# Kernel tuning notes

Hardware: AMD Instinct MI355X
Metric: run time of the kernel (lower is better)

Reference implementation:

```python
import jax, jax.numpy as jnp
import numpy as np

N_NODES = 50000
N_EDGES = 800000
IN_C = 128
OUT_C = 128
EDGE_F = 16
NEG_SLOPE = 0.2
BN_EPS = 1e-5


def setup_inputs() -> dict:
    key = jax.random.key(0)
    ks = jax.random.split(key, 8)
    x = jax.random.normal(ks[0], (N_NODES, IN_C), dtype=jnp.float32)
    edge_index = jax.random.randint(ks[1], (2, N_EDGES), 0, N_NODES, dtype=jnp.int64)
    edge_attr = jax.random.normal(ks[2], (N_EDGES, EDGE_F), dtype=jnp.float32)
    W = jax.random.normal(ks[3], (IN_C, OUT_C), dtype=jnp.float32) / np.sqrt(IN_C)
    att_src = jax.random.normal(ks[4], (OUT_C,), dtype=jnp.float32) / np.sqrt(OUT_C)
    att_dst = jax.random.normal(ks[5], (OUT_C,), dtype=jnp.float32) / np.sqrt(OUT_C)
    bias = jnp.zeros((OUT_C,), dtype=jnp.float32)
    gamma = jnp.ones((OUT_C,), dtype=jnp.float32)
    beta = jnp.zeros((OUT_C,), dtype=jnp.float32)
    return {"x": x, "edge_index": edge_index, "edge_attr": edge_attr, "W": W,
            "att_src": att_src, "att_dst": att_dst, "bias": bias,
            "gamma": gamma, "beta": beta}


def reference(x, edge_index, edge_attr, W, att_src, att_dst, bias, gamma, beta):
    # GATConv, heads=1, concat=False; edge_attr is ignored (edge_dim=None in original).
    N = x.shape[0]
    h = x @ W  # [N, C] linear projection (shared lin_src/lin_dst)
    # add self loops (PyG default add_self_loops=True)
    loops = jnp.broadcast_to(jnp.arange(N, dtype=edge_index.dtype)[None, :], (2, N))
    ei = jnp.concatenate([edge_index, loops], axis=1)
    src, dst = ei[0], ei[1]
    a_src = h @ att_src  # [N] per-node source attention logit
    a_dst = h @ att_dst  # [N] per-node target attention logit
    e = jax.nn.leaky_relu(a_src[src] + a_dst[dst], NEG_SLOPE)  # [E+N]
    # segment softmax over edges grouped by destination node
    m = jax.ops.segment_max(e, dst, num_segments=N)  # every node has a self loop -> nonempty
    ex = jnp.exp(e - m[dst])
    denom = jax.ops.segment_sum(ex, dst, num_segments=N)
    alpha = ex / denom[dst]  # [E+N]
    out = jax.ops.segment_sum(alpha[:, None] * h[src], dst, num_segments=N) + bias  # [N, C]
    # NodeLevelBatchNorm in training mode: batch stats over nodes, biased variance
    mean = jnp.mean(out, axis=0)
    var = jnp.mean((out - mean) ** 2, axis=0)
    y = (out - mean) * jax.lax.rsqrt(var + BN_EPS) * gamma + beta
    return jax.nn.relu(y)
```

## Files before the change

kernel.cpp:

```cpp
#include <hip/hip_runtime.h>
#include <hip/hip_bf16.h>

#define NN 50000
#define NE 800000
#define NC 128
#define NEG 0.2f
#define BN_EPS 1e-5f
#define NB 391
#define EPB 2048
#define DEPTH 16
#define CAP 2560
#define GB 391
#define AGGB 2048

typedef unsigned int u32;
typedef unsigned short u16;
typedef short bf16x8 __attribute__((ext_vector_type(8)));
typedef float f32x4 __attribute__((ext_vector_type(4)));

#define OFF_H       0
#define OFF_ACCUM   3200000
#define OFF_ASRC    6400000
#define OFF_ADST    6450000
#define OFF_GCUR    6500000
#define OFF_GSUM    6500512
#define OFF_GSUMSQ  6500640
#define OFF_BEG     6500768
#define OFF_ENDA    6550768
#define OFF_ESRC    6600768
#define OFF_WGT     7601728
#define OFF_BIN     8602688
#define OFF_WB      9603648
#define OFF_PS      9611840
#define OFF_PQ      9873984
#define OFF_WSEND   10136128
#define NZERO       512

__device__ __forceinline__ float leaky(float e) { return (e >= 0.f) ? e : NEG * e; }

__device__ __forceinline__ u16 f2b(float f) {
  union { float f; u32 u; } v; v.f = f;
  u32 u = v.u;
  return (u16)((u + 0x7fffu + ((u >> 16) & 1u)) >> 16);
}
__device__ __forceinline__ float blo(u32 u) {
  union { u32 u; float f; } v; v.u = u << 16; return v.f;
}
__device__ __forceinline__ float bhi(u32 u) {
  union { u32 u; float f; } v; v.u = u & 0xffff0000u; return v.f;
}

__device__ __forceinline__ bool ei_is64(const void* ei_raw) {
  const unsigned long long* p64 = (const unsigned long long*)ei_raw;
  bool is64 = true;
#pragma unroll
  for (int k = 0; k < 8; ++k) is64 = is64 && (p64[k] < (unsigned long long)NN);
  return is64;
}

__global__ __launch_bounds__(256) void k_prep(
    const float* __restrict__ W, u32* __restrict__ Wb32, int* __restrict__ zbase) {
  if (blockIdx.x == 0) {
    for (int i = threadIdx.x; i < NZERO; i += 256) zbase[i] = 0;
  }
  int q = blockIdx.x * 256 + threadIdx.x;
  if (q >= 2048) return;
  int f = q >> 6, l = q & 63;
  int n = f >> 2, s = f & 3;
  int col = 16 * n + (l & 15);
  int kb = 32 * s + 8 * (l >> 4);
#pragma unroll
  for (int j2 = 0; j2 < 4; ++j2) {
    u16 e0 = f2b(W[(kb + 2 * j2) * NC + col]);
    u16 e1 = f2b(W[(kb + 2 * j2 + 1) * NC + col]);
    Wb32[q * 4 + j2] = ((u32)e1 << 16) | e0;
  }
}

__global__ __launch_bounds__(256) void k_gemm_bin(
    const float* __restrict__ x, const u16* __restrict__ Wb,
    const float* __restrict__ attS, const float* __restrict__ attD,
    u16* __restrict__ h, float* __restrict__ a_src, float* __restrict__ a_dst,
    const void* __restrict__ ei_raw, int* __restrict__ gcur, u32* __restrict__ bin) {
  __shared__ int cnt[NB];
  __shared__ u32 buf[NB * DEPTH];
  const int t = threadIdx.x;

  if (blockIdx.x >= GB) {
    for (int i = t; i < NB; i += 256) cnt[i] = 0;
    __syncthreads();
    bool is64 = ei_is64(ei_raw);
    int base = (blockIdx.x - GB) * EPB;
#pragma unroll
    for (int k = 0; k < 8; ++k) {
      int idx = base + k * 256 + t;
      if (idx >= NE) continue;
      int s, d;
      if (is64) {
        s = (int)((const long long*)ei_raw)[idx];
        d = (int)((const long long*)ei_raw)[NE + idx];
      } else {
        s = ((const int*)ei_raw)[idx];
        d = ((const int*)ei_raw)[NE + idx];
      }
      int b = d >> 7;
      u32 pack = (u32)s | ((u32)(d & 127) << 16);
      int p = atomicAdd(&cnt[b], 1);
      if (p < DEPTH) buf[b * DEPTH + p] = pack;
      else {
        int g = atomicAdd(&gcur[b], 1);
        if (g < CAP) bin[b * CAP + g] = pack;
      }
    }
    __syncthreads();
    for (int b = t; b < NB; b += 256) {
      int c = min(cnt[b], DEPTH);
      if (c > 0) {
        int g = atomicAdd(&gcur[b], c);
        int lim = min(c, max(0, CAP - g));
        int gp = b * CAP + g;
#pragma unroll 4
        for (int i = 0; i < lim; ++i) bin[gp + i] = buf[b * DEPTH + i];
      }
    }
    return;
  }

  const int l = t & 63;
  const int r0 = blockIdx.x * 128 + (t >> 6) * 32;
  const int lr = l & 15;
  const int kg = l >> 4;

  f32x4 acc[2][8];
#pragma unroll
  for (int t2 = 0; t2 < 2; ++t2)
#pragma unroll
    for (int n = 0; n < 8; ++n) acc[t2][n] = (f32x4){0.f, 0.f, 0.f, 0.f};

#pragma unroll
  for (int s = 0; s < 4; ++s) {
    bf16x8 bfr[8];
#pragma unroll
    for (int n = 0; n < 8; ++n)
      bfr[n] = *(const bf16x8*)(Wb + ((size_t)((n * 4 + s) * 64 + l)) * 8);

#pragma unroll
    for (int t2 = 0; t2 < 2; ++t2) {
      int arow = r0 + t2 * 16 + lr;
      f32x4 a0 = (f32x4){0.f,0.f,0.f,0.f}, a1 = a0;
      if (arow < NN) {
        const float* xa = x + (size_t)arow * NC + kg * 8 + s * 32;
        a0 = *(const f32x4*)xa;
        a1 = *(const f32x4*)(xa + 4);
      }
      bf16x8 af;
      af[0]=(short)f2b(a0[0]); af[1]=(short)f2b(a0[1]);
      af[2]=(short)f2b(a0[2]); af[3]=(short)f2b(a0[3]);
      af[4]=(short)f2b(a1[0]); af[5]=(short)f2b(a1[1]);
      af[6]=(short)f2b(a1[2]); af[7]=(short)f2b(a1[3]);
#pragma unroll
      for (int n = 0; n < 8; ++n)
        acc[t2][n] = __builtin_amdgcn_mfma_f32_16x16x32_bf16(af, bfr[n], acc[t2][n], 0, 0, 0);
    }
  }

  float attS_r[8], attD_r[8];
#pragma unroll
  for (int n = 0; n < 8; ++n) {
    attS_r[n] = attS[16 * n + lr];
    attD_r[n] = attD[16 * n + lr];
  }
#pragma unroll
  for (int t2 = 0; t2 < 2; ++t2) {
#pragma unroll
    for (int q = 0; q < 4; ++q) {
      int row = r0 + t2 * 16 + kg * 4 + q;
      bool rok = row < NN;
      float sA = 0.f, sD = 0.f;
#pragma unroll
      for (int n = 0; n < 8; ++n) {
        float v = acc[t2][n][q];
        sA += v * attS_r[n];
        sD += v * attD_r[n];
        if (rok) h[(size_t)row * NC + 16 * n + lr] = f2b(v);
      }
      sA += __shfl_xor(sA, 1); sD += __shfl_xor(sD, 1);
      sA += __shfl_xor(sA, 2); sD += __shfl_xor(sD, 2);
      sA += __shfl_xor(sA, 4); sD += __shfl_xor(sD, 4);
      sA += __shfl_xor(sA, 8); sD += __shfl_xor(sD, 8);
      if (lr == 0 && rok) { a_src[row] = sA; a_dst[row] = sD; }
    }
  }
}

__global__ __launch_bounds__(256) void k_build(
    const int* __restrict__ gcur, const u32* __restrict__ bin,
    const float* __restrict__ a_src, const float* __restrict__ a_dst,
    int* __restrict__ begA, int* __restrict__ endA,
    int* __restrict__ esrc, float* __restrict__ wgt) {
  __shared__ int cnt[128], bs[128], cur[128];
  __shared__ float aDl[128];
  int t = threadIdx.x;
  int b = blockIdx.x;
  int nbase = b << 7;
  int nmax = min(128, NN - nbase);
  int ebeg = b * CAP;
  int E = min(gcur[b], CAP);
  if (t < 128) { cnt[t] = 0; if (t < nmax) aDl[t] = a_dst[nbase + t]; }
  __syncthreads();
  for (int i = t; i < E; i += 256)
    atomicAdd(&cnt[bin[ebeg + i] >> 16], 1);
  __syncthreads();
  if (t < 128) bs[t] = cnt[t];
  __syncthreads();
  for (int off = 1; off < 128; off <<= 1) {
    int xv = (t < 128 && t >= off) ? bs[t - off] : 0;
    __syncthreads();
    if (t < 128) bs[t] += xv;
    __syncthreads();
  }
  if (t < 128) {
    int ex = bs[t] - cnt[t];
    bs[t] = ex;
    cur[t] = 0;
    if (t < nmax) {
      begA[nbase + t] = ebeg + ex;
      endA[nbase + t] = ebeg + ex + cnt[t];
    }
  }
  __syncthreads();
  for (int i = t; i < E; i += 256) {
    u32 e = bin[ebeg + i];
    int s = e & 0xFFFF;
    int ld = e >> 16;
    int p = atomicAdd(&cur[ld], 1);
    int pos = ebeg + bs[ld] + p;
    esrc[pos] = s;
    wgt[pos] = __expf(leaky(a_src[s] + aDl[ld]));
  }
}

__global__ __launch_bounds__(256) void k_aggregate(
    const int* __restrict__ begA, const int* __restrict__ endA,
    const int* __restrict__ esrc, const float* __restrict__ wgt,
    const float* __restrict__ a_src, const float* __restrict__ a_dst,
    const u16* __restrict__ h, u32* __restrict__ accum,
    float* __restrict__ partS, float* __restrict__ partQ) {
  int t = threadIdx.x;
  int l = t & 63;
  int wv = t >> 6;
  float cs0 = 0.f, cs1 = 0.f, cq0 = 0.f, cq1 = 0.f;

  for (int d = blockIdx.x * 4 + wv; d < NN; d += AGGB * 4) {
    int beg = begA[d], end = endA[d];

    float2 ac0 = make_float2(0.f, 0.f), ac1 = ac0, ac2 = ac0, ac3 = ac0;
    float wpart = 0.f;

    for (int j0 = beg; j0 < end; j0 += 64) {
      int n = min(64, end - j0);
      int s = 0;
      float w = 0.f;
      if (l < n) {
        s = esrc[j0 + l];
        w = wgt[j0 + l];
        wpart += w;
      }
      int jj = 0;
      for (; jj + 8 <= n; jj += 8) {
        int s0 = __shfl(s, jj),     s1 = __shfl(s, jj + 1);
        int s2 = __shfl(s, jj + 2), s3 = __shfl(s, jj + 3);
        int s4 = __shfl(s, jj + 4), s5 = __shfl(s, jj + 5);
        int s6 = __shfl(s, jj + 6), s7 = __shfl(s, jj + 7);
        float w0 = __shfl(w, jj),     w1 = __shfl(w, jj + 1);
        float w2 = __shfl(w, jj + 2), w3 = __shfl(w, jj + 3);
        float w4 = __shfl(w, jj + 4), w5 = __shfl(w, jj + 5);
        float w6 = __shfl(w, jj + 6), w7 = __shfl(w, jj + 7);
        u32 h0 = *(const u32*)&h[(size_t)s0 * NC + 2 * l];
        u32 h1 = *(const u32*)&h[(size_t)s1 * NC + 2 * l];
        u32 h2 = *(const u32*)&h[(size_t)s2 * NC + 2 * l];
        u32 h3 = *(const u32*)&h[(size_t)s3 * NC + 2 * l];
        u32 h4 = *(const u32*)&h[(size_t)s4 * NC + 2 * l];
        u32 h5 = *(const u32*)&h[(size_t)s5 * NC + 2 * l];
        u32 h6 = *(const u32*)&h[(size_t)s6 * NC + 2 * l];
        u32 h7 = *(const u32*)&h[(size_t)s7 * NC + 2 * l];
        ac0.x += w0 * blo(h0); ac0.y += w0 * bhi(h0);
        ac1.x += w1 * blo(h1); ac1.y += w1 * bhi(h1);
        ac2.x += w2 * blo(h2); ac2.y += w2 * bhi(h2);
        ac3.x += w3 * blo(h3); ac3.y += w3 * bhi(h3);
        ac0.x += w4 * blo(h4); ac0.y += w4 * bhi(h4);
        ac1.x += w5 * blo(h5); ac1.y += w5 * bhi(h5);
        ac2.x += w6 * blo(h6); ac2.y += w6 * bhi(h6);
        ac3.x += w7 * blo(h7); ac3.y += w7 * bhi(h7);
      }
      for (; jj + 4 <= n; jj += 4) {
        int s0 = __shfl(s, jj),     s1 = __shfl(s, jj + 1);
        int s2 = __shfl(s, jj + 2), s3 = __shfl(s, jj + 3);
        float w0 = __shfl(w, jj),     w1 = __shfl(w, jj + 1);
        float w2 = __shfl(w, jj + 2), w3 = __shfl(w, jj + 3);
        u32 h0 = *(const u32*)&h[(size_t)s0 * NC + 2 * l];
        u32 h1 = *(const u32*)&h[(size_t)s1 * NC + 2 * l];
        u32 h2 = *(const u32*)&h[(size_t)s2 * NC + 2 * l];
        u32 h3 = *(const u32*)&h[(size_t)s3 * NC + 2 * l];
        ac0.x += w0 * blo(h0); ac0.y += w0 * bhi(h0);
        ac1.x += w1 * blo(h1); ac1.y += w1 * bhi(h1);
        ac2.x += w2 * blo(h2); ac2.y += w2 * bhi(h2);
        ac3.x += w3 * blo(h3); ac3.y += w3 * bhi(h3);
      }
      for (; jj < n; ++jj) {
        int sj = __shfl(s, jj);
        float wj = __shfl(w, jj);
        u32 hw = *(const u32*)&h[(size_t)sj * NC + 2 * l];
        ac0.x += wj * blo(hw); ac0.y += wj * bhi(hw);
      }
    }

    for (int off = 32; off > 0; off >>= 1) wpart += __shfl_xor(wpart, off);

    float wself = __expf(leaky(a_src[d] + a_dst[d]));
    u32 hw = *(const u32*)&h[(size_t)d * NC + 2 * l];
    float accx = ac0.x + ac1.x + ac2.x + ac3.x + wself * blo(hw);
    float accy = ac0.y + ac1.y + ac2.y + ac3.y + wself * bhi(hw);

    float inv = 1.f / (wpart + wself);
    float ox = accx * inv, oy = accy * inv;
    accum[(size_t)d * 64 + l] = ((u32)f2b(oy) << 16) | f2b(ox);
    cs0 += ox; cs1 += oy;
    cq0 += ox * ox; cq1 += oy * oy;
  }

  __shared__ float2 shS[256], shQ[256];
  shS[t] = make_float2(cs0, cs1);
  shQ[t] = make_float2(cq0, cq1);
  __syncthreads();
  if (t < 64) {
    float2 a = shS[t], b = shQ[t];
#pragma unroll
    for (int g = 1; g < 4; ++g) {
      float2 s2v = shS[g * 64 + t], q2 = shQ[g * 64 + t];
      a.x += s2v.x; a.y += s2v.y;
      b.x += q2.x;  b.y += q2.y;
    }
    partS[blockIdx.x * 128 + 2 * t]     = a.x;
    partS[blockIdx.x * 128 + 2 * t + 1] = a.y;
    partQ[blockIdx.x * 128 + 2 * t]     = b.x;
    partQ[blockIdx.x * 128 + 2 * t + 1] = b.y;
  }
}

__global__ __launch_bounds__(256) void k_stats2(
    const float* __restrict__ partS, const float* __restrict__ partQ,
    float* __restrict__ gsum, float* __restrict__ gsumsq) {
  __shared__ float shw[4];
  int t = threadIdx.x;
  int b = blockIdx.x;
  int c = b & 127;
  const float* src = (b >> 7) ? partQ : partS;
  float a = 0.f;
#pragma unroll
  for (int i = t; i < AGGB; i += 256) a += src[(size_t)i * 128 + c];
  for (int off = 32; off > 0; off >>= 1) a += __shfl_xor(a, off);
  if ((t & 63) == 0) shw[t >> 6] = a;
  __syncthreads();
  if (t == 0) {
    float r = shw[0] + shw[1] + shw[2] + shw[3];
    if (b >> 7) gsumsq[c] = r;
    else        gsum[c] = r;
  }
}

__global__ __launch_bounds__(256) void k_bn(
    const u32* __restrict__ accum, const float* __restrict__ gsum,
    const float* __restrict__ gsumsq, const float* __restrict__ gamma,
    const float* __restrict__ beta, float* __restrict__ out) {
  int i4 = blockIdx.x * 256 + threadIdx.x;
  if (i4 >= NN * NC / 4) return;
  int c4 = (i4 * 4) & 127;
  f32x4 gs = *(const f32x4*)&gsum[c4];
  f32x4 gq = *(const f32x4*)&gsumsq[c4];
  f32x4 ga = *(const f32x4*)&gamma[c4];
  f32x4 be = *(const f32x4*)&beta[c4];
  u32 p0 = accum[(size_t)i4 * 2];
  u32 p1 = accum[(size_t)i4 * 2 + 1];
  f32x4 v = (f32x4){blo(p0), bhi(p0), blo(p1), bhi(p1)};
  f32x4 o;
#pragma unroll
  for (int j = 0; j < 4; ++j) {
    float mean = gs[j] * (1.0f / NN);
    float var = gq[j] * (1.0f / NN) - mean * mean;
    float inv = rsqrtf(var + BN_EPS);
    float y = (v[j] - mean) * inv * ga[j] + be[j];
    o[j] = (y > 0.f) ? y : 0.f;
  }
  *(f32x4*)&out[(size_t)i4 * 4] = o;
}

extern "C" void kernel_launch(void* const* d_in, const int* in_sizes, int n_in,
                              void* d_out, int out_size, void* d_ws, size_t ws_size,
                              hipStream_t stream) {
  const float* x    = (const float*)d_in[0];
  const void*  ei   = d_in[1];
  const float* W    = (const float*)d_in[3];
  const float* attS = (const float*)d_in[4];
  const float* attD = (const float*)d_in[5];
  const float* gamma = (const float*)d_in[7];
  const float* beta  = (const float*)d_in[8];

  float* ws     = (float*)d_ws;
  u16*   h      = (u16*)(ws + OFF_H);
  u32*   accum  = (u32*)(ws + OFF_ACCUM);
  float* a_src  = ws + OFF_ASRC;
  float* a_dst  = ws + OFF_ADST;
  int*   gcur   = (int*)(ws + OFF_GCUR);
  float* gsum   = ws + OFF_GSUM;
  float* gsumsq = ws + OFF_GSUMSQ;
  int*   begA   = (int*)(ws + OFF_BEG);
  int*   endA   = (int*)(ws + OFF_ENDA);
  int*   esrc   = (int*)(ws + OFF_ESRC);
  float* wgt    = ws + OFF_WGT;
  u32*   bin    = (u32*)(ws + OFF_BIN);
  u32*   wb32   = (u32*)(ws + OFF_WB);
  float* partS  = ws + OFF_PS;
  float* partQ  = ws + OFF_PQ;

  const int nbin = (NE + EPB - 1) / EPB;
  k_prep<<<8, 256, 0, stream>>>(W, wb32, gcur);
  k_gemm_bin<<<GB + nbin, 256, 0, stream>>>(x, (const u16*)wb32, attS, attD,
                                            h, a_src, a_dst, ei, gcur, bin);
  k_build<<<NB, 256, 0, stream>>>(gcur, bin, a_src, a_dst, begA, endA, esrc, wgt);
  k_aggregate<<<AGGB, 256, 0, stream>>>(begA, endA, esrc, wgt, a_src, a_dst, h,
                                        accum, partS, partQ);
  k_stats2<<<256, 256, 0, stream>>>(partS, partQ, gsum, gsumsq);
  k_bn<<<(NN * NC / 4 + 255) / 256, 256, 0, stream>>>(accum, gsum, gsumsq, gamma, beta,
                                                      (float*)d_out);
}
```

Measured before the change: 103.3 us.

## Interleave edge src/weight records, fold self-loop and softmax denominator into build

The build kernel now writes interleaved (src, weight) records with the self-loop appended to each node's segment. It also accumulates the per-node weight sum in shared memory and stores its reciprocal. The aggregate kernel then streams the records with uniform (scalar) loads instead of lane loads plus shuffles, and drops the cross-lane reduction and self-loop special case. This adds shared-memory float atomics to the build kernel and extra padded capacity per bin.

Result: faster. 90.93 us (-12.0%).

```diff
diff --git a/kernel.cpp b/kernel.cpp
--- a/kernel.cpp
+++ b/kernel.cpp
@@ -10,6 +10,7 @@
 #define EPB 2048
 #define DEPTH 16
 #define CAP 2560
+#define CAPR 2688
 #define GB 391
 #define AGGB 2048
 
@@ -27,13 +28,13 @@
 #define OFF_GSUMSQ  6500640
 #define OFF_BEG     6500768
 #define OFF_ENDA    6550768
-#define OFF_ESRC    6600768
-#define OFF_WGT     7601728
-#define OFF_BIN     8602688
-#define OFF_WB      9603648
-#define OFF_PS      9611840
-#define OFF_PQ      9873984
-#define OFF_WSEND   10136128
+#define OFF_WINV    6600768
+#define OFF_BIN     6650768
+#define OFF_REC     7651728
+#define OFF_WB      9753744
+#define OFF_PS      9761936
+#define OFF_PQ      10024080
+#define OFF_WSEND   10286224
 #define NZERO       512
 
 __device__ __forceinline__ float leaky(float e) { return (e >= 0.f) ? e : NEG * e; }
@@ -196,17 +197,21 @@
 __global__ __launch_bounds__(256) void k_build(
     const int* __restrict__ gcur, const u32* __restrict__ bin,
     const float* __restrict__ a_src, const float* __restrict__ a_dst,
-    int* __restrict__ begA, int* __restrict__ endA,
-    int* __restrict__ esrc, float* __restrict__ wgt) {
+    int* __restrict__ begA, int* __restrict__ endA, float* __restrict__ winv,
+    u32* __restrict__ rec) {
   __shared__ int cnt[128], bs[128], cur[128];
-  __shared__ float aDl[128];
+  __shared__ float aDl[128], wsh[128];
   int t = threadIdx.x;
   int b = blockIdx.x;
   int nbase = b << 7;
   int nmax = min(128, NN - nbase);
   int ebeg = b * CAP;
+  int rbeg = b * CAPR;
   int E = min(gcur[b], CAP);
-  if (t < 128) { cnt[t] = 0; if (t < nmax) aDl[t] = a_dst[nbase + t]; }
+  if (t < 128) {
+    cnt[t] = 0; wsh[t] = 0.f;
+    if (t < nmax) aDl[t] = a_dst[nbase + t];
+  }
   __syncthreads();
   for (int i = t; i < E; i += 256)
     atomicAdd(&cnt[bin[ebeg + i] >> 16], 1);
@@ -220,13 +225,8 @@
     __syncthreads();
   }
   if (t < 128) {
-    int ex = bs[t] - cnt[t];
-    bs[t] = ex;
+    bs[t] -= cnt[t];
     cur[t] = 0;
-    if (t < nmax) {
-      begA[nbase + t] = ebeg + ex;
-      endA[nbase + t] = ebeg + ex + cnt[t];
-    }
   }
   __syncthreads();
   for (int i = t; i < E; i += 256) {
@@ -234,100 +234,77 @@
     int s = e & 0xFFFF;
     int ld = e >> 16;
     int p = atomicAdd(&cur[ld], 1);
-    int pos = ebeg + bs[ld] + p;
-    esrc[pos] = s;
-    wgt[pos] = __expf(leaky(a_src[s] + aDl[ld]));
+    int pos = rbeg + bs[ld] + ld + p;
+    float w = __expf(leaky(a_src[s] + aDl[ld]));
+    rec[2 * pos] = (u32)s;
+    rec[2 * pos + 1] = __float_as_uint(w);
+    atomicAdd(&wsh[ld], w);
+  }
+  __syncthreads();
+  if (t < nmax) {
+    int node = nbase + t;
+    int bg = rbeg + bs[t] + t;
+    int cn = cnt[t];
+    float wself = __expf(leaky(a_src[node] + aDl[t]));
+    rec[2 * (bg + cn)] = (u32)node;
+    rec[2 * (bg + cn) + 1] = __float_as_uint(wself);
+    begA[node] = bg;
+    endA[node] = bg + cn + 1;
+    winv[node] = 1.f / (wsh[t] + wself);
   }
 }
 
 __global__ __launch_bounds__(256) void k_aggregate(
     const int* __restrict__ begA, const int* __restrict__ endA,
-    const int* __restrict__ esrc, const float* __restrict__ wgt,
-    const float* __restrict__ a_src, const float* __restrict__ a_dst,
+    const u32* __restrict__ rec, const float* __restrict__ winv,
     const u16* __restrict__ h, u32* __restrict__ accum,
     float* __restrict__ partS, float* __restrict__ partQ) {
   int t = threadIdx.x;
   int l = t & 63;
   int wv = t >> 6;
+  const u32* h32 = (const u32*)h;
+  const uint2* rec2 = (const uint2*)rec;
   float cs0 = 0.f, cs1 = 0.f, cq0 = 0.f, cq1 = 0.f;
 
+#define P1(EJ, A)                                                          \
+  {                                                                        \
+    int sj = __builtin_amdgcn_readfirstlane((int)(EJ).x);                  \
+    float wj = __uint_as_float((EJ).y);                                    \
+    u32 g = h32[(size_t)sj * 64 + l];                                      \
+    A.x += wj * blo(g);                                                    \
+    A.y += wj * bhi(g);                                                    \
+  }
+
   for (int d = blockIdx.x * 4 + wv; d < NN; d += AGGB * 4) {
-    int beg = begA[d], end = endA[d];
-
-    float2 ac0 = make_float2(0.f, 0.f), ac1 = ac0, ac2 = ac0, ac3 = ac0;
-    float wpart = 0.f;
-
-    for (int j0 = beg; j0 < end; j0 += 64) {
-      int n = min(64, end - j0);
-      int s = 0;
-      float w = 0.f;
-      if (l < n) {
-        s = esrc[j0 + l];
-        w = wgt[j0 + l];
-        wpart += w;
-      }
-      int jj = 0;
-      for (; jj + 8 <= n; jj += 8) {
-        int s0 = __shfl(s, jj),     s1 = __shfl(s, jj + 1);
-        int s2 = __shfl(s, jj + 2), s3 = __shfl(s, jj + 3);
-        int s4 = __shfl(s, jj + 4), s5 = __shfl(s, jj + 5);
-        int s6 = __shfl(s, jj + 6), s7 = __shfl(s, jj + 7);
-        float w0 = __shfl(w, jj),     w1 = __shfl(w, jj + 1);
-        float w2 = __shfl(w, jj + 2), w3 = __shfl(w, jj + 3);
-        float w4 = __shfl(w, jj + 4), w5 = __shfl(w, jj + 5);
-        float w6 = __shfl(w, jj + 6), w7 = __shfl(w, jj + 7);
-        u32 h0 = *(const u32*)&h[(size_t)s0 * NC + 2 * l];
-        u32 h1 = *(const u32*)&h[(size_t)s1 * NC + 2 * l];
-        u32 h2 = *(const u32*)&h[(size_t)s2 * NC + 2 * l];
-        u32 h3 = *(const u32*)&h[(size_t)s3 * NC + 2 * l];
-        u32 h4 = *(const u32*)&h[(size_t)s4 * NC + 2 * l];
-        u32 h5 = *(const u32*)&h[(size_t)s5 * NC + 2 * l];
-        u32 h6 = *(const u32*)&h[(size_t)s6 * NC + 2 * l];
-        u32 h7 = *(const u32*)&h[(size_t)s7 * NC + 2 * l];
-        ac0.x += w0 * blo(h0); ac0.y += w0 * bhi(h0);
-        ac1.x += w1 * blo(h1); ac1.y += w1 * bhi(h1);
-        ac2.x += w2 * blo(h2); ac2.y += w2 * bhi(h2);
-        ac3.x += w3 * blo(h3); ac3.y += w3 * bhi(h3);
-        ac0.x += w4 * blo(h4); ac0.y += w4 * bhi(h4);
-        ac1.x += w5 * blo(h5); ac1.y += w5 * bhi(h5);
-        ac2.x += w6 * blo(h6); ac2.y += w6 * bhi(h6);
-        ac3.x += w7 * blo(h7); ac3.y += w7 * bhi(h7);
-      }
-      for (; jj + 4 <= n; jj += 4) {
-        int s0 = __shfl(s, jj),     s1 = __shfl(s, jj + 1);
-        int s2 = __shfl(s, jj + 2), s3 = __shfl(s, jj + 3);
-        float w0 = __shfl(w, jj),     w1 = __shfl(w, jj + 1);
-        float w2 = __shfl(w, jj + 2), w3 = __shfl(w, jj + 3);
-        u32 h0 = *(const u32*)&h[(size_t)s0 * NC + 2 * l];
-        u32 h1 = *(const u32*)&h[(size_t)s1 * NC + 2 * l];
-        u32 h2 = *(const u32*)&h[(size_t)s2 * NC + 2 * l];
-        u32 h3 = *(const u32*)&h[(size_t)s3 * NC + 2 * l];
-        ac0.x += w0 * blo(h0); ac0.y += w0 * bhi(h0);
-        ac1.x += w1 * blo(h1); ac1.y += w1 * bhi(h1);
-        ac2.x += w2 * blo(h2); ac2.y += w2 * bhi(h2);
-        ac3.x += w3 * blo(h3); ac3.y += w3 * bhi(h3);
-      }
-      for (; jj < n; ++jj) {
-        int sj = __shfl(s, jj);
-        float wj = __shfl(w, jj);
-        u32 hw = *(const u32*)&h[(size_t)sj * NC + 2 * l];
-        ac0.x += wj * blo(hw); ac0.y += wj * bhi(hw);
-      }
-    }
-
-    for (int off = 32; off > 0; off >>= 1) wpart += __shfl_xor(wpart, off);
-
-    float wself = __expf(leaky(a_src[d] + a_dst[d]));
-    u32 hw = *(const u32*)&h[(size_t)d * NC + 2 * l];
-    float accx = ac0.x + ac1.x + ac2.x + ac3.x + wself * blo(hw);
-    float accy = ac0.y + ac1.y + ac2.y + ac3.y + wself * bhi(hw);
-
-    float inv = 1.f / (wpart + wself);
-    float ox = accx * inv, oy = accy * inv;
+    int beg = __builtin_amdgcn_readfirstlane(begA[d]);
+    int end = __builtin_amdgcn_readfirstlane(endA[d]);
+
+    float2 a0 = make_float2(0.f, 0.f), a1 = a0, a2 = a0, a3 = a0;
+    int j = beg;
+    for (; j + 8 <= end; j += 8) {
+      const uint2* rp = rec2 + j;
+      uint2 e0 = rp[0], e1 = rp[1], e2 = rp[2], e3 = rp[3];
+      uint2 e4 = rp[4], e5 = rp[5], e6 = rp[6], e7 = rp[7];
+      P1(e0, a0) P1(e1, a1) P1(e2, a2) P1(e3, a3)
+      P1(e4, a0) P1(e5, a1) P1(e6, a2) P1(e7, a3)
+    }
+    for (; j + 2 <= end; j += 2) {
+      uint2 e0 = rec2[j], e1 = rec2[j + 1];
+      P1(e0, a0) P1(e1, a1)
+    }
+    if (j < end) {
+      uint2 e0 = rec2[j];
+      P1(e0, a0)
+    }
+
+    float inv = winv[d];
+    float ox = (a0.x + a1.x + a2.x + a3.x) * inv;
+    float oy = (a0.y + a1.y + a2.y + a3.y) * inv;
     accum[(size_t)d * 64 + l] = ((u32)f2b(oy) << 16) | f2b(ox);
     cs0 += ox; cs1 += oy;
     cq0 += ox * ox; cq1 += oy * oy;
   }
+#undef P1
 
   __shared__ float2 shS[256], shQ[256];
   shS[t] = make_float2(cs0, cs1);
@@ -416,9 +393,9 @@
   float* gsumsq = ws + OFF_GSUMSQ;
   int*   begA   = (int*)(ws + OFF_BEG);
   int*   endA   = (int*)(ws + OFF_ENDA);
-  int*   esrc   = (int*)(ws + OFF_ESRC);
-  float* wgt    = ws + OFF_WGT;
+  float* winv   = ws + OFF_WINV;
   u32*   bin    = (u32*)(ws + OFF_BIN);
+  u32*   rec    = (u32*)(ws + OFF_REC);
   u32*   wb32   = (u32*)(ws + OFF_WB);
   float* partS  = ws + OFF_PS;
   float* partQ  = ws + OFF_PQ;
@@ -427,8 +404,8 @@
   k_prep<<<8, 256, 0, stream>>>(W, wb32, gcur);
   k_gemm_bin<<<GB + nbin, 256, 0, stream>>>(x, (const u16*)wb32, attS, attD,
                                             h, a_src, a_dst, ei, gcur, bin);
-  k_build<<<NB, 256, 0, stream>>>(gcur, bin, a_src, a_dst, begA, endA, esrc, wgt);
-  k_aggregate<<<AGGB, 256, 0, stream>>>(begA, endA, esrc, wgt, a_src, a_dst, h,
+  k_build<<<NB, 256, 0, stream>>>(gcur, bin, a_src, a_dst, begA, endA, winv, rec);
+  k_aggregate<<<AGGB, 256, 0, stream>>>(begA, endA, rec, winv, h,
                                         accum, partS, partQ);
   k_stats2<<<256, 256, 0, stream>>>(partS, partQ, gsum, gsumsq);
   k_bn<<<(NN * NC / 4 + 255) / 256, 256, 0, stream>>>(accum, gsum, gsumsq, gamma, beta,
```
